# Optimization experiments

Measured on AMD Instinct MI355X. Metric: run time of the kernel, lower is better.

Reference implementation:

```python
import jax, jax.numpy as jnp
import numpy as np

D_MODEL = 1024
D_FF = 4096
N_HEADS = 16
D_HEAD = D_MODEL // N_HEADS
EPS = 1e-6


def setup_inputs() -> dict:
    key = jax.random.key(0)
    ks = jax.random.split(key, 12)
    B, S = 8, 1024
    s = 1.0 / np.sqrt(D_MODEL)
    inp = {
        "x": jax.random.normal(ks[0], (B, S, D_MODEL), dtype=jnp.float32),
        "mask": jnp.zeros((B, S, S), dtype=bool),
        "gamma1": jnp.ones((D_MODEL,), jnp.float32),
        "beta1": jnp.zeros((D_MODEL,), jnp.float32),
        "Wq": jax.random.normal(ks[1], (D_MODEL, D_MODEL), jnp.float32) * s,
        "bq": jnp.zeros((D_MODEL,), jnp.float32),
        "Wk": jax.random.normal(ks[2], (D_MODEL, D_MODEL), jnp.float32) * s,
        "bk": jnp.zeros((D_MODEL,), jnp.float32),
        "Wv": jax.random.normal(ks[3], (D_MODEL, D_MODEL), jnp.float32) * s,
        "bv": jnp.zeros((D_MODEL,), jnp.float32),
        "Wo": jax.random.normal(ks[4], (D_MODEL, D_MODEL), jnp.float32) * s,
        "bo": jnp.zeros((D_MODEL,), jnp.float32),
        "gamma2": jnp.ones((D_MODEL,), jnp.float32),
        "beta2": jnp.zeros((D_MODEL,), jnp.float32),
        "W1": jax.random.normal(ks[5], (D_MODEL, D_FF), jnp.float32) * s,
        "b1": jnp.zeros((D_FF,), jnp.float32),
        "W2": jax.random.normal(ks[6], (D_FF, D_MODEL), jnp.float32) * (1.0 / np.sqrt(D_FF)),
        "b2": jnp.zeros((D_MODEL,), jnp.float32),
    }
    return inp


def layer_norm(x, gamma, beta):
    mean = jnp.mean(x, axis=-1, keepdims=True)
    var = jnp.mean(jnp.square(x - mean), axis=-1, keepdims=True)  # unbiased=False
    return gamma * (x - mean) / jnp.sqrt(var + EPS) + beta


def mha(x, mask, Wq, bq, Wk, bk, Wv, bv, Wo, bo):
    B, S, _ = x.shape
    # projections: [B,S,D] -> [B,H,S,dh]
    q = (x @ Wq + bq).reshape(B, S, N_HEADS, D_HEAD).transpose(0, 2, 1, 3)
    k = (x @ Wk + bk).reshape(B, S, N_HEADS, D_HEAD).transpose(0, 2, 1, 3)
    v = (x @ Wv + bv).reshape(B, S, N_HEADS, D_HEAD).transpose(0, 2, 1, 3)
    # scores: [B,H,Sq,Sk]
    scores = jnp.einsum("bhqd,bhkd->bhqk", q, k) / np.sqrt(D_HEAD)
    scores = jnp.where(mask[:, None, :, :], -jnp.inf, scores)
    attn = jax.nn.softmax(scores, axis=-1)
    out = jnp.einsum("bhqk,bhkd->bhqd", attn, v)  # [B,H,Sq,dh]
    out = out.transpose(0, 2, 1, 3).reshape(B, S, D_MODEL)
    return out @ Wo + bo


def reference(x, mask, gamma1, beta1, Wq, bq, Wk, bk, Wv, bv, Wo, bo,
              gamma2, beta2, W1, b1, W2, b2):
    # pre-layer-norm variant per source: x = ln1(x); x = x + attn(x); x = ln2(x); x = x + ff(x)
    x = layer_norm(x, gamma1, beta1)
    x = x + mha(x, mask, Wq, bq, Wk, bk, Wv, bv, Wo, bo)
    x = layer_norm(x, gamma2, beta2)
    ff = jax.nn.relu(x @ W1 + b1) @ W2 + b2
    return x + ff
```

## Files before the change

### kernel.cpp

```cpp
#include <hip/hip_runtime.h>
#include <hip/hip_bf16.h>

typedef __bf16 bf16;
typedef __bf16 bf16x8 __attribute__((ext_vector_type(8)));
typedef __bf16 bf16x4 __attribute__((ext_vector_type(4)));
typedef float  f32x4  __attribute__((ext_vector_type(4)));

#define N_HEADS 16
#define D_HEAD  64
#define SEQ     1024
#define BATCH   8
#define MROWS   (BATCH * SEQ)

__device__ __forceinline__ void gld_lds16(const void* g, void* l) {
    __builtin_amdgcn_global_load_lds(
        (const __attribute__((address_space(1))) void*)g,
        (__attribute__((address_space(3))) void*)l, 16, 0, 0);
}

__global__ __launch_bounds__(256)
void wconv_t(const float* __restrict__ W, bf16* __restrict__ Wt, int K, int N)
{
    __shared__ float tile[32][33];
    const int tx = threadIdx.x & 31, ty = threadIdx.x >> 5;
    const int nb = blockIdx.x * 32, kb = blockIdx.y * 32;
    #pragma unroll
    for (int i = 0; i < 4; ++i)
        tile[ty + i * 8][tx] = W[(size_t)(kb + ty + i * 8) * N + nb + tx];
    __syncthreads();
    #pragma unroll
    for (int i = 0; i < 4; ++i)
        Wt[(size_t)(nb + ty + i * 8) * K + kb + tx] = (bf16)tile[tx][ty + i * 8];
}

__global__ __launch_bounds__(256)
void ln_kernel(const float* __restrict__ x, const float* __restrict__ g,
               const float* __restrict__ b, bf16* __restrict__ obf,
               float* __restrict__ of)
{
    const int row = blockIdx.x;
    const int tid = threadIdx.x;
    const float4 v = ((const float4*)(x + (size_t)row * 1024))[tid];
    float s  = v.x + v.y + v.z + v.w;
    float sq = v.x * v.x + v.y * v.y + v.z * v.z + v.w * v.w;
    #pragma unroll
    for (int off = 32; off; off >>= 1) {
        s  += __shfl_down(s, off);
        sq += __shfl_down(sq, off);
    }
    __shared__ float red[8];
    const int wid = tid >> 6, lid = tid & 63;
    if (lid == 0) { red[wid] = s; red[4 + wid] = sq; }
    __syncthreads();
    if (tid == 0) {
        float ts = red[0] + red[1] + red[2] + red[3];
        float tq = red[4] + red[5] + red[6] + red[7];
        float mean = ts * (1.f / 1024.f);
        float var  = tq * (1.f / 1024.f) - mean * mean;
        red[0] = mean;
        red[1] = rsqrtf(var + 1e-6f);
    }
    __syncthreads();
    const float mean = red[0], rstd = red[1];
    const float4 gg = ((const float4*)g)[tid];
    const float4 bb = ((const float4*)b)[tid];
    float y0 = (v.x - mean) * rstd * gg.x + bb.x;
    float y1 = (v.y - mean) * rstd * gg.y + bb.y;
    float y2 = (v.z - mean) * rstd * gg.z + bb.z;
    float y3 = (v.w - mean) * rstd * gg.w + bb.w;
    float4 o; o.x = y0; o.y = y1; o.z = y2; o.w = y3;
    ((float4*)(of + (size_t)row * 1024))[tid] = o;
    bf16x4 ob; ob[0] = (bf16)y0; ob[1] = (bf16)y1; ob[2] = (bf16)y2; ob[3] = (bf16)y3;
    ((bf16x4*)(obf + (size_t)row * 1024))[tid] = ob;
}

template <int EPI>
__global__ __launch_bounds__(256)
void gemm_bt(const bf16* __restrict__ A, const bf16* __restrict__ Bt,
             const float* __restrict__ bias, const float* __restrict__ resid,
             void* __restrict__ Cout, int M, int N, int K)
{
    __shared__ __attribute__((aligned(16))) bf16 a_lds[128 * 32];
    __shared__ __attribute__((aligned(16))) bf16 b_lds[128 * 32];
    const int tid = threadIdx.x;
    const int l = tid & 63, w = tid >> 6;
    const int lo = l & 15, hi = l >> 4;
    const int m0 = blockIdx.y * 128, n0 = blockIdx.x * 128;
    const int wrow = (w >> 1) * 64, wcol = (w & 1) * 64;
    const int srow = tid >> 2;
    const int scol = (tid & 3) * 8;

    f32x4 acc[4][4];
    #pragma unroll
    for (int i = 0; i < 4; ++i)
        #pragma unroll
        for (int j = 0; j < 4; ++j) acc[i][j] = f32x4{0.f, 0.f, 0.f, 0.f};

    const int nkt = K >> 5;
    for (int kt = 0; kt < nkt; ++kt) {
        __syncthreads();
        const bf16* ag = A  + (size_t)(m0 + srow) * K + kt * 32 + scol;
        const bf16* bg = Bt + (size_t)(n0 + srow) * K + kt * 32 + scol;
        gld_lds16(ag,                  &a_lds[srow * 32 + scol]);
        gld_lds16(ag + (size_t)64 * K, &a_lds[(64 + srow) * 32 + scol]);
        gld_lds16(bg,                  &b_lds[srow * 32 + scol]);
        gld_lds16(bg + (size_t)64 * K, &b_lds[(64 + srow) * 32 + scol]);
        asm volatile("s_waitcnt vmcnt(0)" ::: "memory");
        __syncthreads();

        bf16x8 af[4], bfr[4];
        #pragma unroll
        for (int m = 0; m < 4; ++m)
            af[m] = *(const bf16x8*)&a_lds[(wrow + m * 16 + lo) * 32 + hi * 8];
        #pragma unroll
        for (int n = 0; n < 4; ++n)
            bfr[n] = *(const bf16x8*)&b_lds[(wcol + n * 16 + lo) * 32 + hi * 8];
        #pragma unroll
        for (int m = 0; m < 4; ++m)
            #pragma unroll
            for (int n = 0; n < 4; ++n)
                acc[m][n] = __builtin_amdgcn_mfma_f32_16x16x32_bf16(af[m], bfr[n], acc[m][n], 0, 0, 0);
    }

    #pragma unroll
    for (int m = 0; m < 4; ++m) {
        const int Rbase = m0 + wrow + m * 16 + hi * 4;
        #pragma unroll
        for (int n = 0; n < 4; ++n) {
            const int Cc = n0 + wcol + n * 16 + lo;
            const float bv = bias[Cc];
            #pragma unroll
            for (int r = 0; r < 4; ++r) {
                const int Rr = Rbase + r;
                float vv = acc[m][n][r] + bv;
                if (EPI == 0) {
                    const int b_ = Rr >> 10, s_ = Rr & 1023;
                    const int h_ = Cc >> 6,  d_ = Cc & 63;
                    ((bf16*)Cout)[(((size_t)(b_ * 16 + h_) * 1024 + s_) << 6) + d_] = (bf16)vv;
                } else if (EPI == 1) {
                    vv += resid[(size_t)Rr * N + Cc];
                    ((float*)Cout)[(size_t)Rr * N + Cc] = vv;
                } else {
                    vv = fmaxf(vv, 0.f);
                    ((bf16*)Cout)[(size_t)Rr * N + Cc] = (bf16)vv;
                }
            }
        }
    }
}

__global__ __launch_bounds__(256)
void attn_kernel(const bf16* __restrict__ q, const bf16* __restrict__ k,
                 const bf16* __restrict__ v, const unsigned char* __restrict__ mask,
                 bf16* __restrict__ ctx)
{
    __shared__ __attribute__((aligned(16))) bf16 q_lds[64][72];
    __shared__ __attribute__((aligned(16))) bf16 k_lds[64][72];
    __shared__ __attribute__((aligned(16))) bf16 vt_lds[64][72];
    __shared__ __attribute__((aligned(16))) bf16 p_lds[4][16][72];
    __shared__ __attribute__((aligned(16))) unsigned char m_lds[64][64];

    const int qt = blockIdx.x, hh = blockIdx.y, bb = blockIdx.z;
    const int bh = bb * N_HEADS + hh;
    const int tid = threadIdx.x;
    const int w = tid >> 6, l = tid & 63;
    const int lo = l & 15, hi = l >> 4;

    {
        const bf16* qg = q + ((size_t)bh * SEQ + qt * 64) * D_HEAD;
        #pragma unroll
        for (int i = 0; i < 2; ++i) {
            const int e = (i * 256 + tid) * 8;
            const int r = e >> 6, c = e & 63;
            *(uint4*)&q_lds[r][c] = *(const uint4*)(qg + r * 64 + c);
        }
    }

    f32x4 oacc[4];
    float m_r[4], l_r[4];
    #pragma unroll
    for (int i = 0; i < 4; ++i) {
        oacc[i] = f32x4{0.f, 0.f, 0.f, 0.f};
        m_r[i] = -__builtin_inff();
        l_r[i] = 0.f;
    }

    for (int kt = 0; kt < 16; ++kt) {
        __syncthreads();
        const bf16* kg = k + ((size_t)bh * SEQ + kt * 64) * D_HEAD;
        const bf16* vg = v + ((size_t)bh * SEQ + kt * 64) * D_HEAD;
        #pragma unroll
        for (int i = 0; i < 2; ++i) {
            const int e = (i * 256 + tid) * 8;
            const int r = e >> 6, c = e & 63;
            *(uint4*)&k_lds[r][c] = *(const uint4*)(kg + r * 64 + c);
            uint4 tv = *(const uint4*)(vg + r * 64 + c);
            const bf16* pv = (const bf16*)&tv;
            #pragma unroll
            for (int j = 0; j < 8; ++j) vt_lds[c + j][r] = pv[j];
        }
        {
            const int r = tid >> 2, c0 = (tid & 3) * 16;
            *(uint4*)&m_lds[r][c0] =
                *(const uint4*)(mask + ((size_t)bb * SEQ + qt * 64 + r) * SEQ + kt * 64 + c0);
        }
        __syncthreads();

        f32x4 sf[4];
        #pragma unroll
        for (int ct = 0; ct < 4; ++ct) {
            f32x4 sa = f32x4{0.f, 0.f, 0.f, 0.f};
            #pragma unroll
            for (int kk = 0; kk < 2; ++kk) {
                bf16x8 a   = *(const bf16x8*)&q_lds[w * 16 + lo][kk * 32 + hi * 8];
                bf16x8 bfr = *(const bf16x8*)&k_lds[ct * 16 + lo][kk * 32 + hi * 8];
                sa = __builtin_amdgcn_mfma_f32_16x16x32_bf16(a, bfr, sa, 0, 0, 0);
            }
            sf[ct] = sa;
        }

        float pm[4];
        #pragma unroll
        for (int r = 0; r < 4; ++r) {
            #pragma unroll
            for (int ct = 0; ct < 4; ++ct) {
                float sv = sf[ct][r] * 0.125f;
                if (m_lds[w * 16 + hi * 4 + r][ct * 16 + lo]) sv = -__builtin_inff();
                sf[ct][r] = sv;
            }
            float t0 = fmaxf(fmaxf(sf[0][r], sf[1][r]), fmaxf(sf[2][r], sf[3][r]));
            #pragma unroll
            for (int off = 1; off < 16; off <<= 1) t0 = fmaxf(t0, __shfl_xor(t0, off));
            pm[r] = t0;
        }
        float scl[4];
        #pragma unroll
        for (int r = 0; r < 4; ++r) {
            const float mn = fmaxf(m_r[r], pm[r]);
            scl[r] = __expf(m_r[r] - mn);
            m_r[r] = mn;
            float acc_s = 0.f;
            #pragma unroll
            for (int ct = 0; ct < 4; ++ct) {
                const float p = __expf(sf[ct][r] - mn);
                sf[ct][r] = p;
                acc_s += p;
            }
            #pragma unroll
            for (int off = 1; off < 16; off <<= 1) acc_s += __shfl_xor(acc_s, off);
            l_r[r] = l_r[r] * scl[r] + acc_s;
        }
        #pragma unroll
        for (int n = 0; n < 4; ++n)
            #pragma unroll
            for (int r = 0; r < 4; ++r) oacc[n][r] *= scl[r];

        #pragma unroll
        for (int ct = 0; ct < 4; ++ct)
            #pragma unroll
            for (int r = 0; r < 4; ++r)
                p_lds[w][hi * 4 + r][ct * 16 + lo] = (bf16)sf[ct][r];
        asm volatile("s_waitcnt lgkmcnt(0)" ::: "memory");

        #pragma unroll
        for (int n = 0; n < 4; ++n)
            #pragma unroll
            for (int kk = 0; kk < 2; ++kk) {
                bf16x8 a   = *(const bf16x8*)&p_lds[w][lo][kk * 32 + hi * 8];
                bf16x8 bfr = *(const bf16x8*)&vt_lds[n * 16 + lo][kk * 32 + hi * 8];
                oacc[n] = __builtin_amdgcn_mfma_f32_16x16x32_bf16(a, bfr, oacc[n], 0, 0, 0);
            }
    }

    #pragma unroll
    for (int r = 0; r < 4; ++r) {
        const float inv = 1.f / l_r[r];
        const size_t srow = (size_t)bb * SEQ + qt * 64 + w * 16 + hi * 4 + r;
        const size_t base = (srow * N_HEADS + hh) * D_HEAD;
        #pragma unroll
        for (int n = 0; n < 4; ++n)
            ctx[base + n * 16 + lo] = (bf16)(oacc[n][r] * inv);
    }
}

extern "C" void kernel_launch(void* const* d_in, const int* in_sizes, int n_in,
                              void* d_out, int out_size, void* d_ws, size_t ws_size,
                              hipStream_t stream)
{
    const float* x      = (const float*)d_in[0];
    const unsigned char* mask = (const unsigned char*)d_in[1];
    const float* gamma1 = (const float*)d_in[2];
    const float* beta1  = (const float*)d_in[3];
    const float* Wq     = (const float*)d_in[4];
    const float* bq     = (const float*)d_in[5];
    const float* Wk     = (const float*)d_in[6];
    const float* bk     = (const float*)d_in[7];
    const float* Wv     = (const float*)d_in[8];
    const float* bv     = (const float*)d_in[9];
    const float* Wo     = (const float*)d_in[10];
    const float* bo     = (const float*)d_in[11];
    const float* gamma2 = (const float*)d_in[12];
    const float* beta2  = (const float*)d_in[13];
    const float* W1     = (const float*)d_in[14];
    const float* b1     = (const float*)d_in[15];
    const float* W2     = (const float*)d_in[16];
    const float* b2     = (const float*)d_in[17];

    char* ws = (char*)d_ws;
    const size_t MB = 1u << 20;
    bf16* wqt  = (bf16*)(ws + 0 * MB);
    bf16* wkt  = (bf16*)(ws + 2 * MB);
    bf16* wvt  = (bf16*)(ws + 4 * MB);
    bf16* wot  = (bf16*)(ws + 6 * MB);
    bf16* w1t  = (bf16*)(ws + 8 * MB);
    bf16* w2t  = (bf16*)(ws + 16 * MB);
    bf16* xn1b = (bf16*)(ws + 24 * MB);
    float* xn1f = (float*)(ws + 40 * MB);
    bf16* qb   = (bf16*)(ws + 72 * MB);
    bf16* kb_  = (bf16*)(ws + 88 * MB);
    bf16* vb   = (bf16*)(ws + 104 * MB);
    bf16* ctx  = (bf16*)(ws + 120 * MB);
    bf16* hbuf = (bf16*)(ws + 72 * MB);
    bf16* xn2b = (bf16*)(ws + 136 * MB);
    float* xn2f = (float*)(ws + 152 * MB);
    float* x2f = (float*)d_out;

    wconv_t<<<dim3(32, 32),  256, 0, stream>>>(Wq, wqt, 1024, 1024);
    wconv_t<<<dim3(32, 32),  256, 0, stream>>>(Wk, wkt, 1024, 1024);
    wconv_t<<<dim3(32, 32),  256, 0, stream>>>(Wv, wvt, 1024, 1024);
    wconv_t<<<dim3(32, 32),  256, 0, stream>>>(Wo, wot, 1024, 1024);
    wconv_t<<<dim3(128, 32), 256, 0, stream>>>(W1, w1t, 1024, 4096);
    wconv_t<<<dim3(32, 128), 256, 0, stream>>>(W2, w2t, 4096, 1024);

    ln_kernel<<<MROWS, 256, 0, stream>>>(x, gamma1, beta1, xn1b, xn1f);

    gemm_bt<0><<<dim3(8, 64), 256, 0, stream>>>(xn1b, wqt, bq, nullptr, qb,  MROWS, 1024, 1024);
    gemm_bt<0><<<dim3(8, 64), 256, 0, stream>>>(xn1b, wkt, bk, nullptr, kb_, MROWS, 1024, 1024);
    gemm_bt<0><<<dim3(8, 64), 256, 0, stream>>>(xn1b, wvt, bv, nullptr, vb,  MROWS, 1024, 1024);

    attn_kernel<<<dim3(16, 16, 8), 256, 0, stream>>>(qb, kb_, vb, mask, ctx);

    gemm_bt<1><<<dim3(8, 64), 256, 0, stream>>>(ctx, wot, bo, xn1f, x2f, MROWS, 1024, 1024);

    ln_kernel<<<MROWS, 256, 0, stream>>>(x2f, gamma2, beta2, xn2b, xn2f);

    gemm_bt<2><<<dim3(32, 64), 256, 0, stream>>>(xn2b, w1t, b1, nullptr, hbuf, MROWS, 4096, 1024);

    gemm_bt<1><<<dim3(8, 64), 256, 0, stream>>>(hbuf, w2t, b2, xn2f, (float*)d_out, MROWS, 1024, 4096);
}
```

Before: 698.1 us.

## Fuse QKV projections, bit-pack mask, swizzle V-transpose LDS in attention

```diff
diff --git a/kernel.cpp b/kernel.cpp
--- a/kernel.cpp
+++ b/kernel.cpp
@@ -31,6 +31,25 @@
     #pragma unroll
     for (int i = 0; i < 4; ++i)
         Wt[(size_t)(nb + ty + i * 8) * K + kb + tx] = (bf16)tile[tx][ty + i * 8];
+}
+
+__global__ __launch_bounds__(256)
+void bconcat(const float* __restrict__ bq, const float* __restrict__ bk,
+             const float* __restrict__ bv, float* __restrict__ o)
+{
+    const int i = blockIdx.x * 256 + threadIdx.x;
+    if (i < 1024)       o[i] = bq[i];
+    else if (i < 2048)  o[i] = bk[i - 1024];
+    else if (i < 3072)  o[i] = bv[i - 2048];
+}
+
+__global__ __launch_bounds__(256)
+void mask_pack(const unsigned char* __restrict__ m,
+               unsigned long long* __restrict__ bits)
+{
+    const int i = blockIdx.x * 256 + threadIdx.x;
+    unsigned long long b = __ballot(m[i] != 0);
+    if ((threadIdx.x & 63) == 0) bits[i >> 6] = b;
 }
 
 __global__ __launch_bounds__(256)
@@ -135,8 +154,11 @@
                 float vv = acc[m][n][r] + bv;
                 if (EPI == 0) {
                     const int b_ = Rr >> 10, s_ = Rr & 1023;
-                    const int h_ = Cc >> 6,  d_ = Cc & 63;
-                    ((bf16*)Cout)[(((size_t)(b_ * 16 + h_) * 1024 + s_) << 6) + d_] = (bf16)vv;
+                    const int which = Cc >> 10;
+                    const int cc = Cc & 1023;
+                    const int h_ = cc >> 6, d_ = cc & 63;
+                    ((bf16*)Cout)[(size_t)which * ((size_t)MROWS * 1024) +
+                                  (((size_t)(b_ * 16 + h_) * 1024 + s_) << 6) + d_] = (bf16)vv;
                 } else if (EPI == 1) {
                     vv += resid[(size_t)Rr * N + Cc];
                     ((float*)Cout)[(size_t)Rr * N + Cc] = vv;
@@ -151,17 +173,20 @@
 
 __global__ __launch_bounds__(256)
 void attn_kernel(const bf16* __restrict__ q, const bf16* __restrict__ k,
-                 const bf16* __restrict__ v, const unsigned char* __restrict__ mask,
+                 const bf16* __restrict__ v,
+                 const unsigned long long* __restrict__ mbits,
                  bf16* __restrict__ ctx)
 {
     __shared__ __attribute__((aligned(16))) bf16 q_lds[64][72];
     __shared__ __attribute__((aligned(16))) bf16 k_lds[64][72];
     __shared__ __attribute__((aligned(16))) bf16 vt_lds[64][72];
     __shared__ __attribute__((aligned(16))) bf16 p_lds[4][16][72];
-    __shared__ __attribute__((aligned(16))) unsigned char m_lds[64][64];
-
-    const int qt = blockIdx.x, hh = blockIdx.y, bb = blockIdx.z;
-    const int bh = bb * N_HEADS + hh;
+
+    const int id = blockIdx.x;
+    const int swz = (id & 7) * 256 + (id >> 3);
+    const int qt = swz & 15;
+    const int bh = swz >> 4;
+    const int hh = bh & 15, bb = bh >> 4;
     const int tid = threadIdx.x;
     const int w = tid >> 6, l = tid & 63;
     const int lo = l & 15, hi = l >> 4;
@@ -196,13 +221,15 @@
             *(uint4*)&k_lds[r][c] = *(const uint4*)(kg + r * 64 + c);
             uint4 tv = *(const uint4*)(vg + r * 64 + c);
             const bf16* pv = (const bf16*)&tv;
-            #pragma unroll
-            for (int j = 0; j < 8; ++j) vt_lds[c + j][r] = pv[j];
-        }
-        {
-            const int r = tid >> 2, c0 = (tid & 3) * 16;
-            *(uint4*)&m_lds[r][c0] =
-                *(const uint4*)(mask + ((size_t)bb * SEQ + qt * 64 + r) * SEQ + kt * 64 + c0);
+            const int colS = r ^ (((c >> 3) & 7) << 3);
+            #pragma unroll
+            for (int j = 0; j < 8; ++j) vt_lds[c + j][colS] = pv[j];
+        }
+        unsigned long long mb[4];
+        #pragma unroll
+        for (int r = 0; r < 4; ++r) {
+            const int qrow = qt * 64 + w * 16 + hi * 4 + r;
+            mb[r] = mbits[((((size_t)bb << 10) | qrow) << 4) + kt];
         }
         __syncthreads();
 
@@ -225,7 +252,7 @@
             #pragma unroll
             for (int ct = 0; ct < 4; ++ct) {
                 float sv = sf[ct][r] * 0.125f;
-                if (m_lds[w * 16 + hi * 4 + r][ct * 16 + lo]) sv = -__builtin_inff();
+                if ((mb[r] >> (ct * 16 + lo)) & 1ull) sv = -__builtin_inff();
                 sf[ct][r] = sv;
             }
             float t0 = fmaxf(fmaxf(sf[0][r], sf[1][r]), fmaxf(sf[2][r], sf[3][r]));
@@ -263,13 +290,15 @@
         asm volatile("s_waitcnt lgkmcnt(0)" ::: "memory");
 
         #pragma unroll
-        for (int n = 0; n < 4; ++n)
+        for (int n = 0; n < 4; ++n) {
+            const int g = (((n * 16 + lo) >> 3) & 7) << 3;
             #pragma unroll
             for (int kk = 0; kk < 2; ++kk) {
                 bf16x8 a   = *(const bf16x8*)&p_lds[w][lo][kk * 32 + hi * 8];
-                bf16x8 bfr = *(const bf16x8*)&vt_lds[n * 16 + lo][kk * 32 + hi * 8];
+                bf16x8 bfr = *(const bf16x8*)&vt_lds[n * 16 + lo][(kk * 32 + hi * 8) ^ g];
                 oacc[n] = __builtin_amdgcn_mfma_f32_16x16x32_bf16(a, bfr, oacc[n], 0, 0, 0);
             }
+        }
     }
 
     #pragma unroll
@@ -308,38 +337,38 @@
 
     char* ws = (char*)d_ws;
     const size_t MB = 1u << 20;
-    bf16* wqt  = (bf16*)(ws + 0 * MB);
-    bf16* wkt  = (bf16*)(ws + 2 * MB);
-    bf16* wvt  = (bf16*)(ws + 4 * MB);
+    bf16* wqkv = (bf16*)(ws + 0 * MB);
     bf16* wot  = (bf16*)(ws + 6 * MB);
     bf16* w1t  = (bf16*)(ws + 8 * MB);
     bf16* w2t  = (bf16*)(ws + 16 * MB);
+    unsigned long long* mbits = (unsigned long long*)(ws + 16 * MB);
+    float* bqkv = (float*)(ws + 17 * MB);
     bf16* xn1b = (bf16*)(ws + 24 * MB);
     float* xn1f = (float*)(ws + 40 * MB);
-    bf16* qb   = (bf16*)(ws + 72 * MB);
-    bf16* kb_  = (bf16*)(ws + 88 * MB);
-    bf16* vb   = (bf16*)(ws + 104 * MB);
+    bf16* qkv  = (bf16*)(ws + 72 * MB);
     bf16* ctx  = (bf16*)(ws + 120 * MB);
     bf16* hbuf = (bf16*)(ws + 72 * MB);
     bf16* xn2b = (bf16*)(ws + 136 * MB);
     float* xn2f = (float*)(ws + 152 * MB);
     float* x2f = (float*)d_out;
 
-    wconv_t<<<dim3(32, 32),  256, 0, stream>>>(Wq, wqt, 1024, 1024);
-    wconv_t<<<dim3(32, 32),  256, 0, stream>>>(Wk, wkt, 1024, 1024);
-    wconv_t<<<dim3(32, 32),  256, 0, stream>>>(Wv, wvt, 1024, 1024);
+    wconv_t<<<dim3(32, 32),  256, 0, stream>>>(Wq, wqkv,               1024, 1024);
+    wconv_t<<<dim3(32, 32),  256, 0, stream>>>(Wk, wqkv + 1024 * 1024, 1024, 1024);
+    wconv_t<<<dim3(32, 32),  256, 0, stream>>>(Wv, wqkv + 2048 * 1024, 1024, 1024);
     wconv_t<<<dim3(32, 32),  256, 0, stream>>>(Wo, wot, 1024, 1024);
     wconv_t<<<dim3(128, 32), 256, 0, stream>>>(W1, w1t, 1024, 4096);
+    bconcat<<<12, 256, 0, stream>>>(bq, bk, bv, bqkv);
+    mask_pack<<<32768, 256, 0, stream>>>(mask, mbits);
+
+    ln_kernel<<<MROWS, 256, 0, stream>>>(x, gamma1, beta1, xn1b, xn1f);
+
+    gemm_bt<0><<<dim3(24, 64), 256, 0, stream>>>(xn1b, wqkv, bqkv, nullptr, qkv, MROWS, 3072, 1024);
+
+    attn_kernel<<<2048, 256, 0, stream>>>(qkv, qkv + (size_t)MROWS * 1024,
+                                          qkv + (size_t)2 * MROWS * 1024, mbits, ctx);
+
     wconv_t<<<dim3(32, 128), 256, 0, stream>>>(W2, w2t, 4096, 1024);
 
-    ln_kernel<<<MROWS, 256, 0, stream>>>(x, gamma1, beta1, xn1b, xn1f);
-
-    gemm_bt<0><<<dim3(8, 64), 256, 0, stream>>>(xn1b, wqt, bq, nullptr, qb,  MROWS, 1024, 1024);
-    gemm_bt<0><<<dim3(8, 64), 256, 0, stream>>>(xn1b, wkt, bk, nullptr, kb_, MROWS, 1024, 1024);
-    gemm_bt<0><<<dim3(8, 64), 256, 0, stream>>>(xn1b, wvt, bv, nullptr, vb,  MROWS, 1024, 1024);
-
-    attn_kernel<<<dim3(16, 16, 8), 256, 0, stream>>>(qb, kb_, vb, mask, ctx);
-
     gemm_bt<1><<<dim3(8, 64), 256, 0, stream>>>(ctx, wot, bo, xn1f, x2f, MROWS, 1024, 1024);
 
     ln_kernel<<<MROWS, 256, 0, stream>>>(x2f, gamma2, beta2, xn2b, xn2f);
```

Result: faster. 661.0 us (-5.3%).
